# Optimization experiments

Measured on AMD Instinct MI355X. Metric: run time of the kernel, lower is better.

Reference implementation:

```python
import jax, jax.numpy as jnp
import numpy as np

NUM_HEADS = 16
HEAD_DIM = 80
HIDDEN = NUM_HEADS * HEAD_DIM  # 1280
SEQ = 4096
INV_SCALE = 1.0 / np.sqrt(HEAD_DIM)


def setup_inputs() -> dict:
    key = jax.random.key(0)
    ks = jax.random.split(key, 6)
    return {
        "x": jax.random.normal(ks[0], (SEQ, HIDDEN), dtype=jnp.float32),
        "cos_emb": jax.random.uniform(ks[1], (SEQ, HEAD_DIM), dtype=jnp.float32),
        "sin_emb": jax.random.uniform(ks[2], (SEQ, HEAD_DIM), dtype=jnp.float32),
        "w_qkv": jax.random.normal(ks[3], (HIDDEN, 3 * HIDDEN), dtype=jnp.float32) * (1.0 / np.sqrt(HIDDEN)),
        "b_qkv": jnp.zeros((3 * HIDDEN,), dtype=jnp.float32),
        "w_proj": jax.random.normal(ks[4], (HIDDEN, HIDDEN), dtype=jnp.float32) * (1.0 / np.sqrt(HIDDEN)),
        "b_proj": jnp.zeros((HIDDEN,), dtype=jnp.float32),
    }


def _apply_rotary(t, cos_emb, sin_emb):
    # t: (seq, heads, head_dim); cos/sin: (seq, head_dim) -> broadcast over heads
    c = cos_emb[:, None, :]
    s = sin_emb[:, None, :]
    half = HEAD_DIM // 2
    t1, t2 = t[..., :half], t[..., half:]
    rotated = jnp.concatenate([-t2, t1], axis=-1)
    return t * c + rotated * s


def reference(x, cos_emb, sin_emb, w_qkv, b_qkv, w_proj, b_proj):
    seq_len = x.shape[0]
    qkv = x @ w_qkv + b_qkv  # (S, 3*H)
    qkv = qkv.reshape(seq_len, 3, NUM_HEADS, HEAD_DIM)
    q, k, v = qkv[:, 0], qkv[:, 1], qkv[:, 2]  # each (S, nh, hd)
    q = _apply_rotary(q, cos_emb, sin_emb)
    k = _apply_rotary(k, cos_emb, sin_emb)
    # full (non-causal) attention per head; softmax in float32 as in source
    scores = jnp.einsum("ihd,jhd->hij", q, k) * INV_SCALE
    probs = jax.nn.softmax(scores.astype(jnp.float32), axis=-1).astype(x.dtype)
    out = jnp.einsum("hij,jhd->ihd", probs, v)  # (S, nh, hd)
    out = out.reshape(seq_len, HIDDEN)
    return out @ w_proj + b_proj
```

## Files before the change

### kernel.cpp

```cpp
#include <hip/hip_runtime.h>
#include <hip/hip_bf16.h>

#define SEQ 4096
#define HIDDEN 1280
#define NH 16
#define HD 80
#define QKV_N 3840
#define INV_SCALE 0.11180339887498949f
#define LOG2E 1.4426950408889634f

typedef __attribute__((ext_vector_type(8))) short bf16x8;
typedef __attribute__((ext_vector_type(4))) float f32x4;

__device__ __forceinline__ ushort f2bf(float f) {
  union { float f; unsigned u; } v; v.f = f;
  unsigned u = v.u;
  u += 0x7fff + ((u >> 16) & 1);
  return (ushort)(u >> 16);
}
__device__ __forceinline__ float bf2f(ushort h) {
  union { unsigned u; float f; } v; v.u = ((unsigned)h) << 16;
  return v.f;
}
__device__ __forceinline__ unsigned pk_bf16(float a, float b) {
  union { __hip_bfloat162 h; unsigned u; } v;
  v.h = __float22bfloat162_rn(make_float2(a, b));
  return v.u;
}
__device__ __forceinline__ void async16(void* lds, const void* g) {
  __builtin_amdgcn_global_load_lds(
      (const __attribute__((address_space(1))) unsigned*)g,
      (__attribute__((address_space(3))) unsigned*)(unsigned)(size_t)lds,
      16, 0, 0);
}

__global__ __launch_bounds__(256)
void split_rows(const float* __restrict__ A, ushort* __restrict__ hi,
                ushort* __restrict__ lo, int n) {
  int i = (blockIdx.x * 256 + threadIdx.x) * 4;
  if (i >= n) return;
  float4 v = *(const float4*)&A[i];
  ushort h[4], l[4];
  float x[4] = {v.x, v.y, v.z, v.w};
#pragma unroll
  for (int t = 0; t < 4; ++t) {
    h[t] = f2bf(x[t]);
    l[t] = f2bf(x[t] - bf2f(h[t]));
  }
  *(ushort4*)&hi[i] = *(ushort4*)h;
  if (lo) *(ushort4*)&lo[i] = *(ushort4*)l;
}

__global__ __launch_bounds__(256)
void split_T(const float* __restrict__ W, ushort* __restrict__ hiT,
             ushort* __restrict__ loT, int K, int N) {
  __shared__ float T[32][33];
  const int k0 = blockIdx.y * 32, n0 = blockIdx.x * 32;
  for (int e = threadIdx.x; e < 1024; e += 256) {
    int r = e >> 5, c = e & 31;
    T[r][c] = W[(size_t)(k0 + r) * N + n0 + c];
  }
  __syncthreads();
  for (int e = threadIdx.x; e < 1024; e += 256) {
    int r = e >> 5, c = e & 31;
    float x = T[c][r];
    ushort h = f2bf(x);
    size_t idx = (size_t)(n0 + r) * K + k0 + c;
    hiT[idx] = h;
    if (loT) loT[idx] = f2bf(x - bf2f(h));
  }
}

__global__ __launch_bounds__(256)
void gemm_bt_bf16(const ushort* __restrict__ Ab, const ushort* __restrict__ Bb,
                  const float* __restrict__ bias, float* __restrict__ C,
                  int M, int N, int K) {
  __shared__ __align__(16) ushort lds[16384];
  const int tid = threadIdx.x, lane = tid & 63, w = tid >> 6;
  const int m15 = lane & 15, g = lane >> 4;
  const int m0 = blockIdx.y * 128, n0 = blockIdx.x * 128;
  const int wm = (w & 1) * 64, wn = (w >> 1) * 64;

  const ushort* stage_base =
      (w < 2) ? Ab + (size_t)m0 * K + (w & 1) * 32
              : Bb + (size_t)n0 * K + (w & 1) * 32;
  char* ldsb = (char*)lds;

  f32x4 acc[4][4];
#pragma unroll
  for (int i = 0; i < 4; ++i)
#pragma unroll
    for (int j = 0; j < 4; ++j) acc[i][j] = (f32x4){0.f, 0.f, 0.f, 0.f};

  for (int k0 = 0; k0 < K; k0 += 64) {
    __syncthreads();
#pragma unroll
    for (int i = 0; i < 8; ++i) {
      int o = i * 1024 + lane * 16;
      int row = o >> 6, colb = o & 63;
      async16(ldsb + w * 8192 + o,
              (const char*)(stage_base + (size_t)row * K + k0) + colb);
    }
    __syncthreads();
    bf16x8 ah[4][2], bh[4][2];
#pragma unroll
    for (int t = 0; t < 4; ++t) {
      ah[t][0] = *(const bf16x8*)&lds[(wm + t * 16 + m15) * 32 + g * 8];
      ah[t][1] = *(const bf16x8*)&lds[4096 + (wm + t * 16 + m15) * 32 + g * 8];
      bh[t][0] = *(const bf16x8*)&lds[8192 + (wn + t * 16 + m15) * 32 + g * 8];
      bh[t][1] = *(const bf16x8*)&lds[12288 + (wn + t * 16 + m15) * 32 + g * 8];
    }
#pragma unroll
    for (int mi = 0; mi < 4; ++mi)
#pragma unroll
      for (int ni = 0; ni < 4; ++ni) {
        acc[mi][ni] = __builtin_amdgcn_mfma_f32_16x16x32_bf16(ah[mi][0], bh[ni][0], acc[mi][ni], 0, 0, 0);
        acc[mi][ni] = __builtin_amdgcn_mfma_f32_16x16x32_bf16(ah[mi][1], bh[ni][1], acc[mi][ni], 0, 0, 0);
      }
  }
#pragma unroll
  for (int mi = 0; mi < 4; ++mi)
#pragma unroll
    for (int ni = 0; ni < 4; ++ni) {
      int col = n0 + wn + ni * 16 + m15;
      float bv = bias[col];
#pragma unroll
      for (int r = 0; r < 4; ++r)
        C[(size_t)(m0 + wm + mi * 16 + g * 4 + r) * N + col] = acc[mi][ni][r] + bv;
    }
}

__global__ __launch_bounds__(256)
void gemm_bt_split(const ushort* __restrict__ Ah, const ushort* __restrict__ Al,
                   const ushort* __restrict__ Bh, const ushort* __restrict__ Bl,
                   const float* __restrict__ bias, float* __restrict__ C,
                   int M, int N, int K) {
  __shared__ __align__(16) ushort lds[16384];
  const int tid = threadIdx.x, lane = tid & 63, w = tid >> 6;
  const int m15 = lane & 15, g = lane >> 4;
  const int m0 = blockIdx.y * 128, n0 = blockIdx.x * 128;
  const int wm = (w & 1) * 64, wn = (w >> 1) * 64;

  const ushort* stage_base =
      (w == 0) ? Ah + (size_t)m0 * K :
      (w == 1) ? Al + (size_t)m0 * K :
      (w == 2) ? Bh + (size_t)n0 * K : Bl + (size_t)n0 * K;
  char* ldsb = (char*)lds;

  f32x4 acc[4][4];
#pragma unroll
  for (int i = 0; i < 4; ++i)
#pragma unroll
    for (int j = 0; j < 4; ++j) acc[i][j] = (f32x4){0.f, 0.f, 0.f, 0.f};

  for (int k0 = 0; k0 < K; k0 += 32) {
    __syncthreads();
#pragma unroll
    for (int i = 0; i < 8; ++i) {
      int o = i * 1024 + lane * 16;
      int row = o >> 6, colb = o & 63;
      async16(ldsb + w * 8192 + o,
              (const char*)(stage_base + (size_t)row * K + k0) + colb);
    }
    __syncthreads();
    bf16x8 ah[4], al[4], bh[4], bl[4];
#pragma unroll
    for (int t = 0; t < 4; ++t) {
      ah[t] = *(const bf16x8*)&lds[(wm + t * 16 + m15) * 32 + g * 8];
      al[t] = *(const bf16x8*)&lds[4096 + (wm + t * 16 + m15) * 32 + g * 8];
      bh[t] = *(const bf16x8*)&lds[8192 + (wn + t * 16 + m15) * 32 + g * 8];
      bl[t] = *(const bf16x8*)&lds[12288 + (wn + t * 16 + m15) * 32 + g * 8];
    }
#pragma unroll
    for (int mi = 0; mi < 4; ++mi)
#pragma unroll
      for (int ni = 0; ni < 4; ++ni) {
        acc[mi][ni] = __builtin_amdgcn_mfma_f32_16x16x32_bf16(ah[mi], bh[ni], acc[mi][ni], 0, 0, 0);
        acc[mi][ni] = __builtin_amdgcn_mfma_f32_16x16x32_bf16(ah[mi], bl[ni], acc[mi][ni], 0, 0, 0);
        acc[mi][ni] = __builtin_amdgcn_mfma_f32_16x16x32_bf16(al[mi], bh[ni], acc[mi][ni], 0, 0, 0);
      }
  }
#pragma unroll
  for (int mi = 0; mi < 4; ++mi)
#pragma unroll
    for (int ni = 0; ni < 4; ++ni) {
      int col = n0 + wn + ni * 16 + m15;
      float bv = bias[col];
#pragma unroll
      for (int r = 0; r < 4; ++r)
        C[(size_t)(m0 + wm + mi * 16 + g * 4 + r) * N + col] = acc[mi][ni][r] + bv;
    }
}

__global__ __launch_bounds__(256)
void rotary_qk(const float* __restrict__ qkv, const float* __restrict__ cosb,
               const float* __restrict__ sinb, ushort* __restrict__ Qb,
               ushort* __restrict__ Kb) {
  int id = blockIdx.x * 256 + threadIdx.x;
  int j = id % 48;
  int h = (id / 48) % NH;
  int s = id / (48 * NH);
  size_t qrow = (size_t)((h << 12) + s) * 96;
  if (j < 40) {
    size_t base = (size_t)s * QKV_N + h * HD;
    float c1 = cosb[s * HD + j],      s1 = sinb[s * HD + j];
    float c2 = cosb[s * HD + j + 40], s2 = sinb[s * HD + j + 40];
    const float QS = INV_SCALE * LOG2E;
    float q1 = qkv[base + j], q2 = qkv[base + j + 40];
    Qb[qrow + j]      = f2bf((q1 * c1 - q2 * s1) * QS);
    Qb[qrow + j + 40] = f2bf((q2 * c2 + q1 * s2) * QS);
    float k1 = qkv[base + HIDDEN + j], k2 = qkv[base + HIDDEN + j + 40];
    Kb[qrow + j]      = f2bf(k1 * c1 - k2 * s1);
    Kb[qrow + j + 40] = f2bf(k2 * c2 + k1 * s2);
  } else {
    int d = 80 + (j - 40) * 2;
    Qb[qrow + d] = 0; Qb[qrow + d + 1] = 0;
    Kb[qrow + d] = 0; Kb[qrow + d + 1] = 0;
  }
}

__global__ __launch_bounds__(256)
void v_trans(const float* __restrict__ qkv, ushort* __restrict__ VbT) {
  __shared__ float T[64][81];
  const int h = blockIdx.y, s0 = blockIdx.x * 64;
  for (int e = threadIdx.x; e < 5120; e += 256) {
    int r = e / 80, d = e % 80;
    T[r][d] = qkv[(size_t)(s0 + r) * QKV_N + 2 * HIDDEN + h * HD + d];
  }
  __syncthreads();
  for (int e = threadIdx.x; e < 2560; e += 256) {
    int d = e >> 5, rp = (e & 31) * 2;
    ushort2 p;
    p.x = f2bf(T[rp][d]);
    p.y = f2bf(T[rp + 1][d]);
    *(ushort2*)&VbT[(size_t)h * 80 * SEQ + (size_t)d * SEQ + s0 + rp] = p;
  }
}

#define LPS 88
#define LKS 104
#define LVS 88
__global__ __launch_bounds__(256, 2)
void attn_mfma(const ushort* __restrict__ Qb, const ushort* __restrict__ Kb,
               const ushort* __restrict__ VbT, float* __restrict__ Op,
               float* __restrict__ lp) {
  __shared__ __align__(16) ushort lds[39936];
  ushort* Ps = lds;
  char* ldsb = (char*)lds;

  const int tid = threadIdx.x, lane = tid & 63, w = tid >> 6;
  const int m15 = lane & 15, g = lane >> 4;
  const int h = blockIdx.y, q0 = blockIdx.x * 128, half = blockIdx.z;
  const size_t hq = (size_t)h * SEQ * 96;
  const ushort* Qg = Qb + hq + (size_t)q0 * 96;
  const char* Kg = (const char*)(Kb + hq);
  const ushort* Vg = VbT + (size_t)h * 80 * SEQ;

  bf16x8 qf[2][3];
#pragma unroll
  for (int mi = 0; mi < 2; ++mi)
#pragma unroll
    for (int c = 0; c < 3; ++c)
      qf[mi][c] = *(const bf16x8*)&Qg[(w * 32 + mi * 16 + m15) * 96 + c * 32 + g * 8];

  const char* sbase[7];
  int sstride[7];
#pragma unroll
  for (int i = 0; i < 7; ++i) {
    int c = tid + i * 256;
    if (c < 832) {
      int r = c / 13, cc = c - r * 13;
      sbase[i] = Kg + r * 192 + (cc == 12 ? 176 : cc * 16);
      sstride[i] = 192;
    } else if (c < 1712) {
      int cv = c - 832;
      int r = cv / 11, cc = cv - r * 11;
      sbase[i] = (const char*)(Vg + (size_t)r * SEQ) + (cc >= 8 ? 112 : cc * 16);
      sstride[i] = 2;
    } else {
      sbase[i] = Kg;
      sstride[i] = 192;
    }
  }
  const int dbase = 22528 + tid * 16;

  {
    const size_t kb0 = (size_t)(half * (SEQ / 2));
#pragma unroll
    for (int i = 0; i < 7; ++i)
      async16(ldsb + dbase + i * 4096, sbase[i] + kb0 * sstride[i]);
  }

  f32x4 o_[2][5];
#pragma unroll
  for (int mi = 0; mi < 2; ++mi)
#pragma unroll
    for (int n = 0; n < 5; ++n) o_[mi][n] = (f32x4){0.f, 0.f, 0.f, 0.f};
  float l_part[2] = {0.f, 0.f};

  const int NT = SEQ / 128;
  for (int kt = 0; kt < NT; ++kt) {
    const int cur = kt & 1;
    {
      const size_t kn = (size_t)(half * (SEQ / 2) + ((kt + 1 < NT) ? kt + 1 : kt) * 64);
      const int db = dbase + (cur ^ 1) * 28672;
#pragma unroll
      for (int i = 0; i < 7; ++i)
        async16(ldsb + db + i * 4096, sbase[i] + kn * sstride[i]);
    }
    asm volatile("s_waitcnt vmcnt(7)" ::: "memory");
    __builtin_amdgcn_s_barrier();
    __builtin_amdgcn_sched_barrier(0);

    ushort* Ks = lds + 11264 + cur * 14336;
    ushort* Vt = Ks + 6656;

    f32x4 st[2][4];
#pragma unroll
    for (int mi = 0; mi < 2; ++mi)
#pragma unroll
      for (int j = 0; j < 4; ++j) st[mi][j] = (f32x4){0.f, 0.f, 0.f, 0.f};
#pragma unroll
    for (int j = 0; j < 4; ++j)
#pragma unroll
      for (int c = 0; c < 3; ++c) {
        bf16x8 kf = *(const bf16x8*)&Ks[(j * 16 + m15) * LKS + c * 32 + g * 8];
        st[0][j] = __builtin_amdgcn_mfma_f32_16x16x32_bf16(kf, qf[0][c], st[0][j], 0, 0, 0);
        st[1][j] = __builtin_amdgcn_mfma_f32_16x16x32_bf16(kf, qf[1][c], st[1][j], 0, 0, 0);
      }
#pragma unroll
    for (int mi = 0; mi < 2; ++mi) {
      float ls = 0.f;
#pragma unroll
      for (int j = 0; j < 4; ++j) {
        float p0 = __builtin_amdgcn_exp2f(st[mi][j][0]);
        float p1 = __builtin_amdgcn_exp2f(st[mi][j][1]);
        float p2 = __builtin_amdgcn_exp2f(st[mi][j][2]);
        float p3 = __builtin_amdgcn_exp2f(st[mi][j][3]);
        ls += (p0 + p1) + (p2 + p3);
        uint2 pw;
        pw.x = pk_bf16(p0, p1);
        pw.y = pk_bf16(p2, p3);
        *(uint2*)&Ps[(w * 32 + mi * 16 + m15) * LPS + j * 16 + g * 4] = pw;
      }
      l_part[mi] += ls;
    }
    asm volatile("s_waitcnt lgkmcnt(0)" ::: "memory");
#pragma unroll
    for (int kc = 0; kc < 2; ++kc) {
      bf16x8 pf0 = *(const bf16x8*)&Ps[(w * 32 + m15) * LPS + kc * 32 + g * 8];
      bf16x8 pf1 = *(const bf16x8*)&Ps[(w * 32 + 16 + m15) * LPS + kc * 32 + g * 8];
#pragma unroll
      for (int n = 0; n < 5; ++n) {
        bf16x8 vf = *(const bf16x8*)&Vt[(n * 16 + m15) * LVS + kc * 32 + g * 8];
        o_[0][n] = __builtin_amdgcn_mfma_f32_16x16x32_bf16(pf0, vf, o_[0][n], 0, 0, 0);
        o_[1][n] = __builtin_amdgcn_mfma_f32_16x16x32_bf16(pf1, vf, o_[1][n], 0, 0, 0);
      }
    }
    __builtin_amdgcn_s_barrier();
    __builtin_amdgcn_sched_barrier(0);
  }
  float l_red[2];
#pragma unroll
  for (int mi = 0; mi < 2; ++mi) {
    float t = l_part[mi];
    t += __shfl_xor(t, 16);
    t += __shfl_xor(t, 32);
    l_red[mi] = t;
  }
  if (g == 0) {
    lp[(size_t)half * SEQ * NH + (size_t)(q0 + w * 32 + m15) * NH + h] = l_red[0];
    lp[(size_t)half * SEQ * NH + (size_t)(q0 + w * 32 + 16 + m15) * NH + h] = l_red[1];
  }
  float* Oph = Op + (size_t)half * SEQ * HIDDEN;
#pragma unroll
  for (int mi = 0; mi < 2; ++mi)
#pragma unroll
    for (int r = 0; r < 4; ++r) {
      int grow = q0 + w * 32 + mi * 16 + g * 4 + r;
#pragma unroll
      for (int n = 0; n < 5; ++n)
        Oph[(size_t)grow * HIDDEN + h * HD + n * 16 + m15] = o_[mi][n][r];
    }
}

__global__ __launch_bounds__(256)
void merge_split(const float* __restrict__ Op, const float* __restrict__ lp,
                 ushort* __restrict__ ao_hi, ushort* __restrict__ ao_lo) {
  int id = blockIdx.x * 256 + threadIdx.x;
  int i4 = id * 4;
  int s = i4 / HIDDEN, col = i4 % HIDDEN, hh = col / HD;
  float4 a = *(const float4*)&Op[i4];
  float4 b = *(const float4*)&Op[(size_t)SEQ * HIDDEN + i4];
  float l = lp[s * NH + hh] + lp[SEQ * NH + s * NH + hh];
  float inv = 1.f / l;
  float x[4] = {(a.x + b.x) * inv, (a.y + b.y) * inv,
                (a.z + b.z) * inv, (a.w + b.w) * inv};
  ushort h[4], lo[4];
#pragma unroll
  for (int t = 0; t < 4; ++t) {
    h[t] = f2bf(x[t]);
    lo[t] = f2bf(x[t] - bf2f(h[t]));
  }
  *(ushort4*)&ao_hi[i4] = *(ushort4*)h;
  *(ushort4*)&ao_lo[i4] = *(ushort4*)lo;
}

extern "C" void kernel_launch(void* const* d_in, const int* in_sizes, int n_in,
                              void* d_out, int out_size, void* d_ws, size_t ws_size,
                              hipStream_t stream) {
  const float* x      = (const float*)d_in[0];
  const float* cosb   = (const float*)d_in[1];
  const float* sinb   = (const float*)d_in[2];
  const float* w_qkv  = (const float*)d_in[3];
  const float* b_qkv  = (const float*)d_in[4];
  const float* w_proj = (const float*)d_in[5];
  const float* b_proj = (const float*)d_in[6];
  float* out = (float*)d_out;

  char* ws = (char*)d_ws;
  float*  qkv   = (float*)ws;
  float*  Op    = (float*)ws;
  float*  lp    = (float*)(ws + 41943040);
  ushort* ao_hi = (ushort*)(ws + 42467328);
  ushort* ao_lo = (ushort*)(ws + 52953088);
  size_t o = 62914560;
  ushort* xhi = (ushort*)(ws + o);
  ushort* Qb  = (ushort*)(ws + o);
  o += 20971520;
  ushort* wqT_h = (ushort*)(ws + o);
  ushort* Kb    = (ushort*)(ws + o);
  o += 19660800;
  ushort* VbT   = (ushort*)(ws + o); o += 10485760;
  ushort* wpT_h = (ushort*)(ws + o); o += 3276800;
  ushort* wpT_l = (ushort*)(ws + o);

  split_rows<<<SEQ * HIDDEN / 1024, 256, 0, stream>>>(x, xhi, nullptr, SEQ * HIDDEN);
  split_T<<<dim3(QKV_N / 32, HIDDEN / 32), 256, 0, stream>>>(w_qkv, wqT_h, nullptr, HIDDEN, QKV_N);
  split_T<<<dim3(HIDDEN / 32, HIDDEN / 32), 256, 0, stream>>>(w_proj, wpT_h, wpT_l, HIDDEN, HIDDEN);
  gemm_bt_bf16<<<dim3(QKV_N / 128, SEQ / 128), 256, 0, stream>>>(
      xhi, wqT_h, b_qkv, qkv, SEQ, QKV_N, HIDDEN);
  rotary_qk<<<SEQ * NH * 48 / 256, 256, 0, stream>>>(qkv, cosb, sinb, Qb, Kb);
  v_trans<<<dim3(SEQ / 64, NH), 256, 0, stream>>>(qkv, VbT);
  attn_mfma<<<dim3(SEQ / 128, NH, 2), 256, 0, stream>>>(Qb, Kb, VbT, Op, lp);
  merge_split<<<SEQ * HIDDEN / 1024, 256, 0, stream>>>(Op, lp, ao_hi, ao_lo);
  gemm_bt_split<<<dim3(HIDDEN / 128, SEQ / 128), 256, 0, stream>>>(
      ao_hi, ao_lo, wpT_h, wpT_l, b_proj, out, SEQ, HIDDEN, HIDDEN);
}
```

Before: 376.3 us.

## Double-buffer LDS tiles in both GEMM kernels to overlap loads with MFMA

Result: faster. 365.8 us (-2.8%).

```diff
diff --git a/kernel.cpp b/kernel.cpp
--- a/kernel.cpp
+++ b/kernel.cpp
@@ -71,11 +71,11 @@
   }
 }
 
-__global__ __launch_bounds__(256)
+__global__ __launch_bounds__(256, 2)
 void gemm_bt_bf16(const ushort* __restrict__ Ab, const ushort* __restrict__ Bb,
                   const float* __restrict__ bias, float* __restrict__ C,
                   int M, int N, int K) {
-  __shared__ __align__(16) ushort lds[16384];
+  __shared__ __align__(16) ushort lds[32768];
   const int tid = threadIdx.x, lane = tid & 63, w = tid >> 6;
   const int m15 = lane & 15, g = lane >> 4;
   const int m0 = blockIdx.y * 128, n0 = blockIdx.x * 128;
@@ -86,29 +86,45 @@
               : Bb + (size_t)n0 * K + (w & 1) * 32;
   char* ldsb = (char*)lds;
 
+  float bv[4];
+#pragma unroll
+  for (int ni = 0; ni < 4; ++ni) bv[ni] = bias[n0 + wn + ni * 16 + m15];
+
   f32x4 acc[4][4];
 #pragma unroll
   for (int i = 0; i < 4; ++i)
 #pragma unroll
     for (int j = 0; j < 4; ++j) acc[i][j] = (f32x4){0.f, 0.f, 0.f, 0.f};
 
-  for (int k0 = 0; k0 < K; k0 += 64) {
-    __syncthreads();
+  const int NK = K >> 6;
+#pragma unroll
+  for (int i = 0; i < 8; ++i) {
+    int o = i * 1024 + lane * 16;
+    int row = o >> 6, colb = o & 63;
+    async16(ldsb + w * 8192 + o, (const char*)(stage_base + (size_t)row * K) + colb);
+  }
+  for (int it = 0; it < NK; ++it) {
+    const int cur = it & 1;
+    const int kn = ((it + 1 < NK) ? it + 1 : it) * 64;
 #pragma unroll
     for (int i = 0; i < 8; ++i) {
       int o = i * 1024 + lane * 16;
       int row = o >> 6, colb = o & 63;
-      async16(ldsb + w * 8192 + o,
-              (const char*)(stage_base + (size_t)row * K + k0) + colb);
-    }
-    __syncthreads();
+      async16(ldsb + (cur ^ 1) * 32768 + w * 8192 + o,
+              (const char*)(stage_base + (size_t)row * K + kn) + colb);
+    }
+    asm volatile("s_waitcnt vmcnt(8)" ::: "memory");
+    __builtin_amdgcn_s_barrier();
+    __builtin_amdgcn_sched_barrier(0);
+
+    const ushort* L = lds + cur * 16384;
     bf16x8 ah[4][2], bh[4][2];
 #pragma unroll
     for (int t = 0; t < 4; ++t) {
-      ah[t][0] = *(const bf16x8*)&lds[(wm + t * 16 + m15) * 32 + g * 8];
-      ah[t][1] = *(const bf16x8*)&lds[4096 + (wm + t * 16 + m15) * 32 + g * 8];
-      bh[t][0] = *(const bf16x8*)&lds[8192 + (wn + t * 16 + m15) * 32 + g * 8];
-      bh[t][1] = *(const bf16x8*)&lds[12288 + (wn + t * 16 + m15) * 32 + g * 8];
+      ah[t][0] = *(const bf16x8*)&L[(wm + t * 16 + m15) * 32 + g * 8];
+      ah[t][1] = *(const bf16x8*)&L[4096 + (wm + t * 16 + m15) * 32 + g * 8];
+      bh[t][0] = *(const bf16x8*)&L[8192 + (wn + t * 16 + m15) * 32 + g * 8];
+      bh[t][1] = *(const bf16x8*)&L[12288 + (wn + t * 16 + m15) * 32 + g * 8];
     }
 #pragma unroll
     for (int mi = 0; mi < 4; ++mi)
@@ -117,25 +133,26 @@
         acc[mi][ni] = __builtin_amdgcn_mfma_f32_16x16x32_bf16(ah[mi][0], bh[ni][0], acc[mi][ni], 0, 0, 0);
         acc[mi][ni] = __builtin_amdgcn_mfma_f32_16x16x32_bf16(ah[mi][1], bh[ni][1], acc[mi][ni], 0, 0, 0);
       }
+    __builtin_amdgcn_s_barrier();
+    __builtin_amdgcn_sched_barrier(0);
   }
 #pragma unroll
   for (int mi = 0; mi < 4; ++mi)
 #pragma unroll
     for (int ni = 0; ni < 4; ++ni) {
       int col = n0 + wn + ni * 16 + m15;
-      float bv = bias[col];
 #pragma unroll
       for (int r = 0; r < 4; ++r)
-        C[(size_t)(m0 + wm + mi * 16 + g * 4 + r) * N + col] = acc[mi][ni][r] + bv;
-    }
-}
-
-__global__ __launch_bounds__(256)
+        C[(size_t)(m0 + wm + mi * 16 + g * 4 + r) * N + col] = acc[mi][ni][r] + bv[ni];
+    }
+}
+
+__global__ __launch_bounds__(256, 2)
 void gemm_bt_split(const ushort* __restrict__ Ah, const ushort* __restrict__ Al,
                    const ushort* __restrict__ Bh, const ushort* __restrict__ Bl,
                    const float* __restrict__ bias, float* __restrict__ C,
                    int M, int N, int K) {
-  __shared__ __align__(16) ushort lds[16384];
+  __shared__ __align__(16) ushort lds[32768];
   const int tid = threadIdx.x, lane = tid & 63, w = tid >> 6;
   const int m15 = lane & 15, g = lane >> 4;
   const int m0 = blockIdx.y * 128, n0 = blockIdx.x * 128;
@@ -147,29 +164,45 @@
       (w == 2) ? Bh + (size_t)n0 * K : Bl + (size_t)n0 * K;
   char* ldsb = (char*)lds;
 
+  float bv[4];
+#pragma unroll
+  for (int ni = 0; ni < 4; ++ni) bv[ni] = bias[n0 + wn + ni * 16 + m15];
+
   f32x4 acc[4][4];
 #pragma unroll
   for (int i = 0; i < 4; ++i)
 #pragma unroll
     for (int j = 0; j < 4; ++j) acc[i][j] = (f32x4){0.f, 0.f, 0.f, 0.f};
 
-  for (int k0 = 0; k0 < K; k0 += 32) {
-    __syncthreads();
+  const int NK = K >> 5;
+#pragma unroll
+  for (int i = 0; i < 8; ++i) {
+    int o = i * 1024 + lane * 16;
+    int row = o >> 6, colb = o & 63;
+    async16(ldsb + w * 8192 + o, (const char*)(stage_base + (size_t)row * K) + colb);
+  }
+  for (int it = 0; it < NK; ++it) {
+    const int cur = it & 1;
+    const int kn = ((it + 1 < NK) ? it + 1 : it) * 32;
 #pragma unroll
     for (int i = 0; i < 8; ++i) {
       int o = i * 1024 + lane * 16;
       int row = o >> 6, colb = o & 63;
-      async16(ldsb + w * 8192 + o,
-              (const char*)(stage_base + (size_t)row * K + k0) + colb);
-    }
-    __syncthreads();
+      async16(ldsb + (cur ^ 1) * 32768 + w * 8192 + o,
+              (const char*)(stage_base + (size_t)row * K + kn) + colb);
+    }
+    asm volatile("s_waitcnt vmcnt(8)" ::: "memory");
+    __builtin_amdgcn_s_barrier();
+    __builtin_amdgcn_sched_barrier(0);
+
+    const ushort* L = lds + cur * 16384;
     bf16x8 ah[4], al[4], bh[4], bl[4];
 #pragma unroll
     for (int t = 0; t < 4; ++t) {
-      ah[t] = *(const bf16x8*)&lds[(wm + t * 16 + m15) * 32 + g * 8];
-      al[t] = *(const bf16x8*)&lds[4096 + (wm + t * 16 + m15) * 32 + g * 8];
-      bh[t] = *(const bf16x8*)&lds[8192 + (wn + t * 16 + m15) * 32 + g * 8];
-      bl[t] = *(const bf16x8*)&lds[12288 + (wn + t * 16 + m15) * 32 + g * 8];
+      ah[t] = *(const bf16x8*)&L[(wm + t * 16 + m15) * 32 + g * 8];
+      al[t] = *(const bf16x8*)&L[4096 + (wm + t * 16 + m15) * 32 + g * 8];
+      bh[t] = *(const bf16x8*)&L[8192 + (wn + t * 16 + m15) * 32 + g * 8];
+      bl[t] = *(const bf16x8*)&L[12288 + (wn + t * 16 + m15) * 32 + g * 8];
     }
 #pragma unroll
     for (int mi = 0; mi < 4; ++mi)
@@ -179,16 +212,17 @@
         acc[mi][ni] = __builtin_amdgcn_mfma_f32_16x16x32_bf16(ah[mi], bl[ni], acc[mi][ni], 0, 0, 0);
         acc[mi][ni] = __builtin_amdgcn_mfma_f32_16x16x32_bf16(al[mi], bh[ni], acc[mi][ni], 0, 0, 0);
       }
+    __builtin_amdgcn_s_barrier();
+    __builtin_amdgcn_sched_barrier(0);
   }
 #pragma unroll
   for (int mi = 0; mi < 4; ++mi)
 #pragma unroll
     for (int ni = 0; ni < 4; ++ni) {
       int col = n0 + wn + ni * 16 + m15;
-      float bv = bias[col];
 #pragma unroll
       for (int r = 0; r < 4; ++r)
-        C[(size_t)(m0 + wm + mi * 16 + g * 4 + r) * N + col] = acc[mi][ni][r] + bv;
+        C[(size_t)(m0 + wm + mi * 16 + g * 4 + r) * N + col] = acc[mi][ni][r] + bv[ni];
     }
 }
 
```
